# Optimization experiments

Hardware: AMD Instinct MI355X
Metric: run time of the kernel (lower is better)

## Reference

```python
import jax, jax.numpy as jnp
import numpy as np


def _sig_scores(n, queries, keys, scale, corr):
    # queries/keys: [B, L, H, E]
    B, L_Q, H, E = queries.shape
    L_K = keys.shape[1]
    q = jnp.transpose(queries, (0, 2, 1, 3))  # [B,H,L_Q,E]
    k = jnp.transpose(keys, (0, 2, 1, 3))     # [B,H,L_K,E]
    if corr:
        # FFT autocorrelation along the time axis (torch irfft default n = L for even L)
        qf = jnp.fft.rfft(jnp.transpose(queries, (0, 2, 3, 1)), axis=-1)  # [B,H,E,Lf]
        kf = jnp.fft.rfft(jnp.transpose(keys, (0, 2, 3, 1)), axis=-1)
        ac = jnp.fft.irfft(qf * jnp.conj(kf), n=L_Q, axis=-1)             # [B,H,E,L]
        ac = jnp.transpose(ac, (0, 1, 3, 2))                              # [B,H,L,E]
    else:
        ac = q
    amp = jnp.linalg.norm(ac, axis=-1)          # [B,H,L_Q]
    _, top_idx = jax.lax.top_k(amp, n)          # [B,H,n]
    q_sel = jnp.take_along_axis(q, top_idx[..., None], axis=2)  # [B,H,n,E]
    scores = jnp.einsum('bhnd,bhmd->bhnm', q_sel, k) * scale    # [B,H,n,L_K]
    full = jnp.full((B, H, L_Q, L_K), -jnp.inf, dtype=queries.dtype)
    b_ix = jnp.arange(B)[:, None, None]
    h_ix = jnp.arange(H)[None, :, None]
    full = full.at[b_ix, h_ix, top_idx].set(scores)             # scatter rows at top_idx
    return jnp.transpose(full, (0, 1, 3, 2))                    # [B,H,L_K,L_Q]


def setup_inputs() -> dict:
    key = jax.random.key(0)
    ks = jax.random.split(key, 6)
    B, L, H, E = 2, 1024, 8, 64
    tf_queries = jax.random.normal(ks[0], (B, L, H, E), dtype=jnp.float32)
    queries = jax.random.normal(ks[1], (B, L, H, E), dtype=jnp.float32)
    keys = jax.random.normal(ks[2], (B, L, H, E), dtype=jnp.float32)
    values = jax.random.normal(ks[3], (B, L, H, E), dtype=jnp.float32)
    mask = jnp.zeros((1,), dtype=bool)  # unused by the module
    # nn.Linear(2*L, L): weight [L, 2L], bias [L]
    transform_w = jax.random.normal(ks[4], (L, 2 * L), dtype=jnp.float32) / np.sqrt(2 * L)
    transform_b = jax.random.normal(ks[5], (L,), dtype=jnp.float32) * 0.01
    return {"tf_queries": tf_queries, "queries": queries, "keys": keys,
            "values": values, "mask": mask,
            "transform_w": transform_w, "transform_b": transform_b}


def reference(tf_queries, queries, keys, values, mask, transform_w, transform_b):
    B, L, H, E = queries.shape
    scale = 1.0 / np.sqrt(E)  # out_channels == E
    n_top = min(int(5 * np.ceil(np.log(L))), L)
    attn_t = _sig_scores(n_top, queries, keys, scale, corr=1)        # [B,H,L,L]
    attn_tf = _sig_scores(n_top, tf_queries, tf_queries, scale, corr=0)
    cat = jnp.concatenate([attn_t, attn_tf], axis=-1)                # [B,H,L,2L]
    cat = jax.nn.softmax(cat, axis=-1)
    # Linear(2L -> L); dropout is identity in eval mode
    final_attn = cat @ transform_w.T + transform_b                   # [B,H,L,L]
    out = jnp.einsum('bhlm,bhmd->bhld', final_attn,
                     jnp.transpose(values, (0, 2, 1, 3)))            # [B,H,L,E]
    return jnp.transpose(out, (0, 2, 1, 3))                          # [B,L,H,E]
```

## Files before the change

kernel.cpp:

```cpp
#include <hip/hip_runtime.h>


#define NTOP 35
#define NJ 70
#define LLMIN (-0x7FFFFFFFFFFFFFFFLL - 1)

static __device__ __forceinline__ void fma4(float4& a, float4 q, float4 k) {
  a.x = fmaf(q.x,k.x,a.x); a.y = fmaf(q.y,k.y,a.y);
  a.z = fmaf(q.z,k.z,a.z); a.w = fmaf(q.w,k.w,a.w);
}

static __device__ __forceinline__ void wave_top35(const float* vals, int* out) {
  int lane = threadIdx.x;
  long long kreg[16];
  long long lmax = LLMIN;
  #pragma unroll
  for (int s = 0; s < 16; ++s) {
    int l = (s << 6) + lane;
    long long key = ((long long)(int)__float_as_uint(vals[l]) << 32)
                    | (unsigned int)(1023 - l);
    kreg[s] = key;
    lmax = key > lmax ? key : lmax;
  }
  for (int it = 0; it < NTOP; ++it) {
    long long g = lmax;
    #pragma unroll
    for (int off = 1; off < 64; off <<= 1) {
      long long o = __shfl_xor(g, off);
      g = o > g ? o : g;
    }
    if (lane == 0) out[it] = 1023 - (int)(g & 0xFFFFFFFFLL);
    if (lmax == g) {
      lmax = LLMIN;
      #pragma unroll
      for (int s = 0; s < 16; ++s) {
        if (kreg[s] == g) kreg[s] = LLMIN;
        lmax = kreg[s] > lmax ? kreg[s] : lmax;
      }
    }
  }
}

__global__ __launch_bounds__(512) void d1_prep(
    const float* __restrict__ q, const float* __restrict__ k,
    const float* __restrict__ w,
    float* __restrict__ Wt, float* __restrict__ amp2part) {
  __shared__ float smem[8192];
  int bid = blockIdx.x;
  int tid = threadIdx.x;
  if (bid < 256) {
    int bh = bid & 15;  int eg = bid >> 4;
    int b = bh >> 3, h = bh & 7;
    float4* QP = reinterpret_cast<float4*>(smem);
    float4* Ks = QP + 1024;
    const float* qb  = q + (size_t)b*524288 + h*64 + eg*4;
    const float* kbp = k + (size_t)b*524288 + h*64 + eg*4;
    for (int r = tid; r < 1024; r += 512)
      QP[(r & 7)*128 + (r >> 3)] =
          *reinterpret_cast<const float4*>(qb + (size_t)r*512);
    for (int i = tid; i < 1024; i += 512)
      Ks[i] = *reinterpret_cast<const float4*>(kbp + (size_t)i*512);
    __syncthreads();
    int half = tid >> 8, tg = tid & 255;
    int tb = tg << 2;
    int tstart = half << 9;
    float4 acc[4], wnd[4];
    #pragma unroll
    for (int i = 0; i < 4; ++i) {
      acc[i] = make_float4(0,0,0,0);
      int r = (tstart + tb + i) & 1023;
      wnd[i] = QP[(r & 7)*128 + (r >> 3)];
    }
    for (int t8 = 0; t8 < 512; t8 += 8) {
      #pragma unroll
      for (int s = 0; s < 8; ++s) {
        float4 kv = Ks[tstart + t8 + s];
        #pragma unroll
        for (int i = 0; i < 4; ++i)
          fma4(acc[i], wnd[(s + i) & 3], kv);
        int rn = (tstart + t8 + s + tb + 4) & 1023;
        wnd[s & 3] = QP[(rn & 7)*128 + (rn >> 3)];
      }
    }
    __syncthreads();
    if (half == 1) {
      float* rp = smem + tg*17;
      const float* a = reinterpret_cast<const float*>(acc);
      #pragma unroll
      for (int i = 0; i < 16; ++i) rp[i] = a[i];
    }
    __syncthreads();
    if (half == 0) {
      const float* rp = smem + tg*17;
      float* a = reinterpret_cast<float*>(acc);
      #pragma unroll
      for (int i = 0; i < 16; ++i) a[i] += rp[i];
      float4 r;
      r.x = acc[0].x*acc[0].x + acc[0].y*acc[0].y + acc[0].z*acc[0].z + acc[0].w*acc[0].w;
      r.y = acc[1].x*acc[1].x + acc[1].y*acc[1].y + acc[1].z*acc[1].z + acc[1].w*acc[1].w;
      r.z = acc[2].x*acc[2].x + acc[2].y*acc[2].y + acc[2].z*acc[2].z + acc[2].w*acc[2].w;
      r.w = acc[3].x*acc[3].x + acc[3].y*acc[3].y + acc[3].z*acc[3].z + acc[3].w*acc[3].w;
      *reinterpret_cast<float4*>(amp2part + (((size_t)(bh*16 + eg)) << 10) + tb) = r;
    }
  } else {
    int wid = bid - 256;
    int c0 = (wid & 31) << 6, r0 = (wid >> 5) << 6;
    float* tile = smem;
    #pragma unroll
    for (int s = 0; s < 8; ++s) {
      int idx = tid + (s << 9);
      int r = idx >> 6, c = idx & 63;
      tile[r*65 + c] = w[(size_t)(r0 + r)*2048 + c0 + c];
    }
    __syncthreads();
    #pragma unroll
    for (int s = 0; s < 8; ++s) {
      int idx = tid + (s << 9);
      int c = idx >> 6, r = idx & 63;
      Wt[(size_t)(c0 + c)*1024 + r0 + r] = tile[r*65 + c];
    }
  }
}

__global__ __launch_bounds__(1024) void d2_topk(
    const float* __restrict__ amp2part, const float* __restrict__ tfq,
    int* __restrict__ St, int* __restrict__ Stf) {
  __shared__ float vals[1024];
  int bid = blockIdx.x;
  int tid = threadIdx.x;
  bool isT = bid < 16;
  int bh = isT ? bid : bid - 16;
  if (isT) {
    float s = 0.f;
    #pragma unroll
    for (int eg = 0; eg < 16; ++eg)
      s += amp2part[(((size_t)(bh*16 + eg)) << 10) + tid];
    vals[tid] = s;
  } else {
    int b = bh >> 3, h = bh & 7;
    const float4* p = reinterpret_cast<const float4*>(
        tfq + (((size_t)(b*1024 + tid)*8 + h) << 6));
    float s = 0.f;
    #pragma unroll
    for (int i = 0; i < 16; ++i) {
      float4 vv = p[i];
      s += vv.x*vv.x + vv.y*vv.y + vv.z*vv.z + vv.w*vv.w;
    }
    vals[tid] = s;
  }
  __syncthreads();
  if (tid < 64) wave_top35(vals, (isT ? St : Stf) + bh*40);
}

__global__ __launch_bounds__(256) void d3_mix(
    const float* __restrict__ q, const float* __restrict__ k,
    const float* __restrict__ tfq,
    const float* __restrict__ Wt, const float* __restrict__ bias,
    const float* __restrict__ values,
    const int* __restrict__ St, const int* __restrict__ Stf,
    float* __restrict__ WVp, float* __restrict__ P) {
  __shared__ float4 smbuf[1712];
  float* f = reinterpret_cast<float*>(smbuf);
  int bid = blockIdx.x;
  int tid = threadIdx.x;
  if (bid < 1152) {
    int jq = bid / 64;
    int rem = bid - jq*64;
    int bh = rem >> 2, mc = rem & 3;
    int b = bh >> 3, h = bh & 7;
    int j0 = jq << 2;
    const float* pj[4];
    #pragma unroll
    for (int x = 0; x < 4; ++x) {
      int j = j0 + x;
      if (j < NTOP)      pj[x] = Wt + (size_t)St [bh*40 + j]*1024;
      else if (j < NJ)   pj[x] = Wt + (size_t)(1024 + Stf[bh*40 + j-NTOP])*1024;
      else if (j == NJ)  pj[x] = bias;
      else               pj[x] = Wt;
    }
    int d = tid & 63, mp = tid >> 6;
    int m0 = (mc << 8) + mp;
    float a0=0.f, a1=0.f, a2=0.f, a3=0.f;
    #pragma unroll 16
    for (int i = 0; i < 64; ++i) {
      int m = m0 + (i << 2);
      float vv = values[(((size_t)(b*1024 + m)*8 + h) << 6) + d];
      a0 = fmaf(pj[0][m], vv, a0);
      a1 = fmaf(pj[1][m], vv, a1);
      a2 = fmaf(pj[2][m], vv, a2);
      a3 = fmaf(pj[3][m], vv, a3);
    }
    float4* red = smbuf;
    red[tid] = make_float4(a0, a1, a2, a3);
    __syncthreads();
    int jj = tid >> 6, dd = tid & 63;
    float4 r0 = red[dd], r1 = red[64+dd], r2 = red[128+dd], r3 = red[192+dd];
    float s;
    if (jj == 0)      s = r0.x + r1.x + r2.x + r3.x;
    else if (jj == 1) s = r0.y + r1.y + r2.y + r3.y;
    else if (jj == 2) s = r0.z + r1.z + r2.z + r3.z;
    else              s = r0.w + r1.w + r2.w + r3.w;
    if (j0 + jj > NJ) s = 0.f;
    WVp[(size_t)mc*73728 + ((size_t)bh*72 + j0 + jj)*64 + dd] = s;
  } else {
    int gid = bid - 1152;
    int bh = gid >> 5;  int m0 = (gid & 31) << 5;
    int b = bh >> 3, h = bh & 7;
    float* qs   = f;
    float* ts   = f + 2240;
    float* sc   = f + 4480;
    float* invs = f + 6816;
    for (int i = tid; i < NTOP*64; i += 256) {
      int j = i >> 6, e = i & 63;
      qs[i] = q  [(((size_t)(b*1024 + St [bh*40 + j])*8 + h) << 6) + e];
      ts[i] = tfq[(((size_t)(b*1024 + Stf[bh*40 + j])*8 + h) << 6) + e];
    }
    __syncthreads();
    int mi = tid & 31, g = tid >> 5;
    int br = g >> 2, g4 = g & 3;
    int m = m0 + mi;
    const float* src = br ? tfq : k;
    float4 kr[16];
    const float4* p = reinterpret_cast<const float4*>(
        src + (((size_t)(b*1024 + m)*8 + h) << 6));
    #pragma unroll
    for (int i = 0; i < 16; ++i) kr[i] = p[i];
    const float4* fs4 = reinterpret_cast<const float4*>(br ? ts : qs);
    int sb = br ? NTOP : 0;
    for (int j = g4; j < NTOP; j += 4) {
      float s = 0.f;
      #pragma unroll
      for (int e4 = 0; e4 < 16; ++e4) {
        float4 qv = fs4[j*16 + e4];
        s += qv.x*kr[e4].x + qv.y*kr[e4].y + qv.z*kr[e4].z + qv.w*kr[e4].w;
      }
      sc[mi*73 + sb + j] = s * 0.125f;
    }
    __syncthreads();
    if (tid < 32) {
      float mx = -1e30f;
      for (int j = 0; j < NJ; ++j) mx = fmaxf(mx, sc[tid*73 + j]);
      float sum = 0.f;
      for (int j = 0; j < NJ; ++j) {
        float e = __expf(sc[tid*73 + j] - mx);
        sc[tid*73 + j] = e; sum += e;
      }
      invs[tid] = 1.0f / sum;
    }
    __syncthreads();
    float* Pb = P + ((size_t)bh*1024 + m0)*72;
    for (int i = tid; i < 32*72; i += 256) {
      int mm = i / 72, j = i - mm*72;
      Pb[i] = (j < NJ) ? sc[mm*73 + j] * invs[mm] : 0.f;
    }
  }
}

__global__ __launch_bounds__(256) void k6_out(
    const float* __restrict__ P, const float* __restrict__ WVp,
    float* __restrict__ out) {
  __shared__ float wv[72*64];
  __shared__ float Pl[72*68];
  int bh = blockIdx.x, lc = blockIdx.y;
  int l0 = lc << 6;
  int b = bh >> 3, h = bh & 7;
  int tid = threadIdx.x;
  {
    const float* W0 = WVp + (size_t)bh*4608;
    for (int i = tid; i < 4608; i += 256)
      wv[i] = W0[i] + W0[73728 + i] + W0[147456 + i] + W0[221184 + i];
  }
  {
    const float* Pg = P + ((size_t)bh*1024 + l0)*72;
    for (int i = tid; i < 4608; i += 256) {
      int l = i / 72, j = i - l*72;
      Pl[j*68 + l] = Pg[i];
    }
  }
  __syncthreads();
  int d = tid & 63, lg = tid >> 6;
  int lb = lg << 4;
  float acc[16];
  float base = wv[NJ*64 + d];
  #pragma unroll
  for (int i = 0; i < 16; ++i) acc[i] = base;
  for (int j = 0; j < NJ; ++j) {
    float wvj = wv[j*64 + d];
    const float4* pr = reinterpret_cast<const float4*>(Pl + j*68 + lb);
    float4 p0 = pr[0], p1 = pr[1], p2 = pr[2], p3 = pr[3];
    acc[0]  = fmaf(p0.x, wvj, acc[0]);  acc[1]  = fmaf(p0.y, wvj, acc[1]);
    acc[2]  = fmaf(p0.z, wvj, acc[2]);  acc[3]  = fmaf(p0.w, wvj, acc[3]);
    acc[4]  = fmaf(p1.x, wvj, acc[4]);  acc[5]  = fmaf(p1.y, wvj, acc[5]);
    acc[6]  = fmaf(p1.z, wvj, acc[6]);  acc[7]  = fmaf(p1.w, wvj, acc[7]);
    acc[8]  = fmaf(p2.x, wvj, acc[8]);  acc[9]  = fmaf(p2.y, wvj, acc[9]);
    acc[10] = fmaf(p2.z, wvj, acc[10]); acc[11] = fmaf(p2.w, wvj, acc[11]);
    acc[12] = fmaf(p3.x, wvj, acc[12]); acc[13] = fmaf(p3.y, wvj, acc[13]);
    acc[14] = fmaf(p3.z, wvj, acc[14]); acc[15] = fmaf(p3.w, wvj, acc[15]);
  }
  #pragma unroll
  for (int i = 0; i < 16; ++i) {
    int l = l0 + lb + i;
    out[(((size_t)(b*1024 + l)*8 + h) << 6) + d] = acc[i];
  }
}

extern "C" void kernel_launch(void* const* d_in, const int* in_sizes, int n_in,
                              void* d_out, int out_size, void* d_ws, size_t ws_size,
                              hipStream_t stream) {
  const float* tfq  = (const float*)d_in[0];
  const float* q    = (const float*)d_in[1];
  const float* k    = (const float*)d_in[2];
  const float* v    = (const float*)d_in[3];
  const float* tw   = (const float*)d_in[5];
  const float* tb   = (const float*)d_in[6];
  float* out = (float*)d_out;

  char* ws = (char*)d_ws;
  float* amp2part = (float*)(ws);
  int*   St  = (int*)  (ws + 1048576);
  int*   Stf = (int*)  (ws + 1052672);
  float* Wt  = (float*)(ws + 1056768);
  float* P   = (float*)(ws + 9445376);
  float* WVp = (float*)(ws + 14163968);

  d1_prep<<<768, 512, 0, stream>>>(q, k, tw, Wt, amp2part);
  d2_topk<<<32, 1024, 0, stream>>>(amp2part, tfq, St, Stf);
  d3_mix <<<1664, 256, 0, stream>>>(q, k, tfq, Wt, tb, v, St, Stf, WVp, P);
  k6_out <<<dim3(16, 16), 256, 0, stream>>>(P, WVp, out);
}
```

Before: 201.8 us.

## Use 8-row register windows and a 4-way time split in correlation prep

Reworks the direct circular-correlation loop in the prep kernel. Each thread now accumulates 8 output lags instead of 4, and the 512 threads split the time axis into four chunks instead of two. This doubles the reuse of each key vector loaded from LDS and halves per-thread loop length. A new XOR swizzle sets the query layout in shared memory to avoid bank conflicts. The cost is more registers per thread and a two-stage LDS reduction with extra barriers and a larger shared buffer.

```diff
diff --git a/kernel.cpp b/kernel.cpp
--- a/kernel.cpp
+++ b/kernel.cpp
@@ -41,11 +41,13 @@
   }
 }
 
+static __device__ __forceinline__ int qsw(int r) { return r ^ ((r >> 3) & 7); }
+
 __global__ __launch_bounds__(512) void d1_prep(
     const float* __restrict__ q, const float* __restrict__ k,
     const float* __restrict__ w,
     float* __restrict__ Wt, float* __restrict__ amp2part) {
-  __shared__ float smem[8192];
+  __shared__ float smem[9216];
   int bid = blockIdx.x;
   int tid = threadIdx.x;
   if (bid < 256) {
@@ -55,52 +57,70 @@
     float4* Ks = QP + 1024;
     const float* qb  = q + (size_t)b*524288 + h*64 + eg*4;
     const float* kbp = k + (size_t)b*524288 + h*64 + eg*4;
-    for (int r = tid; r < 1024; r += 512)
-      QP[(r & 7)*128 + (r >> 3)] =
-          *reinterpret_cast<const float4*>(qb + (size_t)r*512);
-    for (int i = tid; i < 1024; i += 512)
-      Ks[i] = *reinterpret_cast<const float4*>(kbp + (size_t)i*512);
-    __syncthreads();
-    int half = tid >> 8, tg = tid & 255;
-    int tb = tg << 2;
-    int tstart = half << 9;
-    float4 acc[4], wnd[4];
-    #pragma unroll
-    for (int i = 0; i < 4; ++i) {
+    for (int r = tid; r < 1024; r += 512) {
+      QP[qsw(r)] = *reinterpret_cast<const float4*>(qb  + (size_t)r*512);
+      Ks[r]      = *reinterpret_cast<const float4*>(kbp + (size_t)r*512);
+    }
+    __syncthreads();
+    int ch = tid >> 7, tg = tid & 127;
+    int tb = tg << 3;
+    int tstart = ch << 8;
+    float4 acc[8], wnd[8];
+    #pragma unroll
+    for (int i = 0; i < 8; ++i) {
       acc[i] = make_float4(0,0,0,0);
       int r = (tstart + tb + i) & 1023;
-      wnd[i] = QP[(r & 7)*128 + (r >> 3)];
-    }
-    for (int t8 = 0; t8 < 512; t8 += 8) {
+      wnd[i] = QP[qsw(r)];
+    }
+    for (int t8 = 0; t8 < 256; t8 += 8) {
       #pragma unroll
       for (int s = 0; s < 8; ++s) {
         float4 kv = Ks[tstart + t8 + s];
         #pragma unroll
-        for (int i = 0; i < 4; ++i)
-          fma4(acc[i], wnd[(s + i) & 3], kv);
-        int rn = (tstart + t8 + s + tb + 4) & 1023;
-        wnd[s & 3] = QP[(rn & 7)*128 + (rn >> 3)];
+        for (int i = 0; i < 8; ++i)
+          fma4(acc[i], wnd[(s + i) & 7], kv);
+        int rn = (tstart + t8 + s + tb + 8) & 1023;
+        wnd[s] = QP[qsw(rn)];
       }
     }
     __syncthreads();
-    if (half == 1) {
-      float* rp = smem + tg*17;
-      const float* a = reinterpret_cast<const float*>(acc);
-      #pragma unroll
-      for (int i = 0; i < 16; ++i) rp[i] = a[i];
-    }
-    __syncthreads();
-    if (half == 0) {
-      const float* rp = smem + tg*17;
-      float* a = reinterpret_cast<float*>(acc);
-      #pragma unroll
-      for (int i = 0; i < 16; ++i) a[i] += rp[i];
-      float4 r;
-      r.x = acc[0].x*acc[0].x + acc[0].y*acc[0].y + acc[0].z*acc[0].z + acc[0].w*acc[0].w;
-      r.y = acc[1].x*acc[1].x + acc[1].y*acc[1].y + acc[1].z*acc[1].z + acc[1].w*acc[1].w;
-      r.z = acc[2].x*acc[2].x + acc[2].y*acc[2].y + acc[2].z*acc[2].z + acc[2].w*acc[2].w;
-      r.w = acc[3].x*acc[3].x + acc[3].y*acc[3].y + acc[3].z*acc[3].z + acc[3].w*acc[3].w;
-      *reinterpret_cast<float4*>(amp2part + (((size_t)(bh*16 + eg)) << 10) + tb) = r;
+    float* bufA = smem;
+    float* bufB = smem + 4608;
+    float* a = reinterpret_cast<float*>(acc);
+    if (ch == 1 || ch == 3) {
+      float* rp = (ch == 1 ? bufA : bufB) + tg*36;
+      #pragma unroll
+      for (int i = 0; i < 32; ++i) rp[i] = a[i];
+    }
+    __syncthreads();
+    if (ch == 0 || ch == 2) {
+      const float* rp = (ch == 0 ? bufA : bufB) + tg*36;
+      #pragma unroll
+      for (int i = 0; i < 32; ++i) a[i] += rp[i];
+    }
+    __syncthreads();
+    if (ch == 2) {
+      float* rp = bufA + tg*36;
+      #pragma unroll
+      for (int i = 0; i < 32; ++i) rp[i] = a[i];
+    }
+    __syncthreads();
+    if (ch == 0) {
+      const float* rp = bufA + tg*36;
+      #pragma unroll
+      for (int i = 0; i < 32; ++i) a[i] += rp[i];
+      float4 r0, r1;
+      r0.x = acc[0].x*acc[0].x + acc[0].y*acc[0].y + acc[0].z*acc[0].z + acc[0].w*acc[0].w;
+      r0.y = acc[1].x*acc[1].x + acc[1].y*acc[1].y + acc[1].z*acc[1].z + acc[1].w*acc[1].w;
+      r0.z = acc[2].x*acc[2].x + acc[2].y*acc[2].y + acc[2].z*acc[2].z + acc[2].w*acc[2].w;
+      r0.w = acc[3].x*acc[3].x + acc[3].y*acc[3].y + acc[3].z*acc[3].z + acc[3].w*acc[3].w;
+      r1.x = acc[4].x*acc[4].x + acc[4].y*acc[4].y + acc[4].z*acc[4].z + acc[4].w*acc[4].w;
+      r1.y = acc[5].x*acc[5].x + acc[5].y*acc[5].y + acc[5].z*acc[5].z + acc[5].w*acc[5].w;
+      r1.z = acc[6].x*acc[6].x + acc[6].y*acc[6].y + acc[6].z*acc[6].z + acc[6].w*acc[6].w;
+      r1.w = acc[7].x*acc[7].x + acc[7].y*acc[7].y + acc[7].z*acc[7].z + acc[7].w*acc[7].w;
+      float4* op = reinterpret_cast<float4*>(
+          amp2part + (((size_t)(bh*16 + eg)) << 10) + tb);
+      op[0] = r0; op[1] = r1;
     }
   } else {
     int wid = bid - 256;
```

Measured after the change: 185.5 us. -8.1%, faster.
